# Kernel tuning notes

Hardware: AMD Instinct MI355X
Metric: run time of the kernel (lower is better)

Reference implementation:

```python
import jax, jax.numpy as jnp
import numpy as np

NY, NU, NHIDDEN = 64, 32, 512
T, BATCH = 512, 256
DAMP = 0.99


def setup_inputs() -> dict:
    key = jax.random.key(0)
    ks = jax.random.split(key, 8)
    nh2 = NHIDDEN // 2
    theta = jax.random.uniform(ks[0], (nh2,)) * (jnp.pi / 2)
    lmbd_real = DAMP * jnp.cos(theta)
    lmbd_imag = DAMP * jnp.sin(theta)
    B = jax.random.normal(ks[1], (NHIDDEN, NU)) / np.sqrt(NU) * np.sqrt(1.0 - DAMP ** 2)
    W_y2x = jax.random.normal(ks[2], (NHIDDEN, NY)) / np.sqrt(NY)
    b_y2x = jnp.zeros((NHIDDEN,), jnp.float32)
    W_x2y = jax.random.normal(ks[3], (NY, NHIDDEN)) / np.sqrt(NHIDDEN)
    b_x2y = jnp.zeros((NY,), jnp.float32)
    y0 = jax.random.normal(ks[4], (BATCH, NY), jnp.float32)
    U = jax.random.normal(ks[5], (T, BATCH, NU), jnp.float32)
    return {"y0": y0, "U": U, "lmbd_real": lmbd_real, "lmbd_imag": lmbd_imag,
            "B": B, "W_y2x": W_y2x, "b_y2x": b_y2x, "W_x2y": W_x2y, "b_x2y": b_x2y}


def reference(y0, U, lmbd_real, lmbd_imag, B, W_y2x, b_y2x, W_x2y, b_x2y):
    # x_{k+1} = x_k @ A^T + B u_k, where A = [[diag(lr), -diag(li)], [diag(li), diag(lr)]]
    # i.e. an elementwise complex rotation of the paired state halves.
    nh2 = lmbd_real.shape[0]
    Bu = jnp.einsum('tbu,hu->tbh', U, B)          # [T, batch, Nhidden]
    x0 = y0 @ W_y2x.T + b_y2x                     # [batch, Nhidden]

    def step(x, bu):
        xr, xi = x[..., :nh2], x[..., nh2:]
        nr = lmbd_real * xr - lmbd_imag * xi
        ni = lmbd_imag * xr + lmbd_real * xi
        xn = jnp.concatenate([nr, ni], axis=-1) + bu
        return xn, xn

    _, Xs = jax.lax.scan(step, x0, Bu)            # [T, batch, Nhidden]
    X = jnp.concatenate([x0[None], Xs], axis=0)   # [T+1, batch, Nhidden]
    Y = X @ W_x2y.T + b_x2y                       # [T+1, batch, Ny]
    return Y
```

## Files before the change

### kernel.cpp

```cpp
#include <hip/hip_runtime.h>


constexpr int NY  = 64;
constexpr int NU  = 32;
constexpr int NH  = 512;
constexpr int NH2 = 256;
constexpr int TT  = 512;
constexpr int BB  = 256;
constexpr int KK  = 16;
constexpr int NSS = TT / KK;

constexpr int USP = 40;
constexpr int BUP = 513;
constexpr int XSP = 520;

typedef __attribute__((ext_vector_type(4))) short sh4;
typedef __attribute__((ext_vector_type(8))) short sh8;
typedef __attribute__((ext_vector_type(4))) float f32x4;

#define MFMA16(a, b, c) __builtin_amdgcn_mfma_f32_16x16x32_bf16((a), (b), (c), 0, 0, 0)
#define CAT8(a, b) __builtin_shufflevector((a), (b), 0, 1, 2, 3, 4, 5, 6, 7)

__device__ __forceinline__ unsigned short bfh(float x) {
    return (unsigned short)(__float_as_uint(x) >> 16);
}
__device__ __forceinline__ float bf2f(unsigned short h) {
    return __uint_as_float(((unsigned)h) << 16);
}

__global__ __launch_bounds__(512, 2)
void lru_fused_kernel(const float* __restrict__ y0,
                      const float* __restrict__ U,
                      const float* __restrict__ lmr,
                      const float* __restrict__ lmi,
                      const float* __restrict__ Bmat,
                      const float* __restrict__ Wy2x,
                      const float* __restrict__ by2x,
                      const float* __restrict__ Wx2y,
                      const float* __restrict__ bx2y,
                      float* __restrict__ Y)
{
    const int b    = blockIdx.x;
    const int tid  = threadIdx.x;
    const int w    = tid >> 6;
    const int l    = tid & 63;
    const int lr16 = l & 15;
    const int lg   = l >> 4;

    __shared__ unsigned short us_h[2][64][USP], us_l[2][64][USP];
    __shared__ float          bu[KK][BUP];
    __shared__ unsigned short xs_h[KK][XSP], xs_l[KK][XSP];
    __shared__ float          psy[8][4][16][17];
    __shared__ float          y0s[NY];

    sh8 whi[4][2], wlo[4][2];
#pragma unroll
    for (int nt = 0; nt < 4; ++nt) {
#pragma unroll
        for (int kk2 = 0; kk2 < 2; ++kk2) {
            sh8 vh, vl;
#pragma unroll
            for (int h2 = 0; h2 < 2; ++h2) {
                const int k0 = (w << 6) + (kk2 << 5) + (h2 << 4) + (lg << 2);
                const int p0 = k0 >> 1;
                const float* Wn = Wx2y + ((nt << 4) + lr16) * NH;
                const float e[4] = { Wn[p0], Wn[p0 + 256], Wn[p0 + 1], Wn[p0 + 257] };
#pragma unroll
                for (int j = 0; j < 4; ++j) {
                    const unsigned short h = bfh(e[j]);
                    vh[h2 * 4 + j] = (short)h;
                    vl[h2 * 4 + j] = (short)bfh(e[j] - bf2f(h));
                }
            }
            whi[nt][kk2] = vh;
            wlo[nt][kk2] = vl;
        }
    }
    sh8 bbh[4], bbl[4];
#pragma unroll
    for (int q = 0; q < 4; ++q) {
        sh8 vh, vl;
#pragma unroll
        for (int h2 = 0; h2 < 2; ++h2) {
            const int hrow = (w << 6) + (q << 4) + lr16;
            const int u0   = (h2 << 4) + (lg << 2);
            const float4 f4 = *reinterpret_cast<const float4*>(&Bmat[hrow * NU + u0]);
            const float e[4] = { f4.x, f4.y, f4.z, f4.w };
#pragma unroll
            for (int j = 0; j < 4; ++j) {
                const unsigned short h = bfh(e[j]);
                vh[h2 * 4 + j] = (short)h;
                vl[h2 * 4 + j] = (short)bfh(e[j] - bf2f(h));
            }
        }
        bbh[q] = vh;
        bbl[q] = vl;
    }
    const float bias = bx2y[l];

    const float4* Ug = reinterpret_cast<const float4*>(U);
    {
        const int i = tid;
        const float4 f = Ug[((i >> 3) * BB + b) * 8 + (i & 7)];
        const int t = i >> 3, c4 = (i & 7) << 2;
        sh4 vh, vl;
        const float e[4] = { f.x, f.y, f.z, f.w };
#pragma unroll
        for (int j = 0; j < 4; ++j) {
            const unsigned short h = bfh(e[j]);
            vh[j] = (short)h;
            vl[j] = (short)bfh(e[j] - bf2f(h));
        }
        *reinterpret_cast<sh4*>(&us_h[0][t][c4]) = vh;
        *reinterpret_cast<sh4*>(&us_l[0][t][c4]) = vl;
    }
    if (tid < NY) y0s[tid] = y0[b * NY + tid];
    __syncthreads();

    float lamr = 0.f, lami = 0.f, xr = 0.f, xi = 0.f;
    if (tid < NH2) {
        lamr = lmr[tid];
        lami = lmi[tid];
        const float* wr = &Wy2x[tid * NY];
        const float* wi = &Wy2x[(NH2 + tid) * NY];
        float a0 = 0, a1 = 0, a2 = 0, a3 = 0;
        float c0 = 0, c1 = 0, c2 = 0, c3 = 0;
#pragma unroll
        for (int y = 0; y < NY; y += 4) {
            a0 += wr[y + 0] * y0s[y + 0];
            a1 += wr[y + 1] * y0s[y + 1];
            a2 += wr[y + 2] * y0s[y + 2];
            a3 += wr[y + 3] * y0s[y + 3];
            c0 += wi[y + 0] * y0s[y + 0];
            c1 += wi[y + 1] * y0s[y + 1];
            c2 += wi[y + 2] * y0s[y + 2];
            c3 += wi[y + 3] * y0s[y + 3];
        }
        xr = by2x[tid]       + (a0 + a1) + (a2 + a3);
        xi = by2x[NH2 + tid] + (c0 + c1) + (c2 + c3);
        const unsigned short hr = bfh(xr), hi2 = bfh(xi);
        reinterpret_cast<unsigned*>(&xs_h[0][0])[tid] = (unsigned)hr | ((unsigned)hi2 << 16);
        reinterpret_cast<unsigned*>(&xs_l[0][0])[tid] =
            (unsigned)bfh(xr - bf2f(hr)) | ((unsigned)bfh(xi - bf2f(hi2)) << 16);
    }
    __syncthreads();

    {
        f32x4 ay[4];
#pragma unroll
        for (int nt = 0; nt < 4; ++nt) ay[nt] = (f32x4){0.f, 0.f, 0.f, 0.f};
#pragma unroll
        for (int kk2 = 0; kk2 < 2; ++kk2) {
            const unsigned short* xp = &xs_h[lr16][(w << 6) + (kk2 << 5) + (lg << 2)];
            const unsigned short* xq = &xs_l[lr16][(w << 6) + (kk2 << 5) + (lg << 2)];
            const sh8 axh = CAT8(*(const sh4*)xp, *(const sh4*)(xp + 16));
            const sh8 axl = CAT8(*(const sh4*)xq, *(const sh4*)(xq + 16));
#pragma unroll
            for (int nt = 0; nt < 4; ++nt) {
                ay[nt] = MFMA16(axh, whi[nt][kk2], ay[nt]);
                ay[nt] = MFMA16(axl, whi[nt][kk2], ay[nt]);
                ay[nt] = MFMA16(axh, wlo[nt][kk2], ay[nt]);
            }
        }
#pragma unroll
        for (int nt = 0; nt < 4; ++nt)
#pragma unroll
            for (int r = 0; r < 4; ++r)
                psy[w][nt][(lg << 2) + r][lr16] = ay[nt][r];
    }
    __syncthreads();
    if (tid < NY) {
        float acc = bias;
#pragma unroll
        for (int w8 = 0; w8 < 8; ++w8) acc += psy[w8][l >> 4][0][l & 15];
        Y[b * NY + l] = acc;
    }

    float4 pf0, pf1;

    for (int st = 0; st < NSS; ++st) {
        const int c   = st >> 2;
        const int q4  = st & 3;
        const int buf = c & 1;

        if (q4 == 0 && c < 7 && tid >= NH2) {
            const int t0g = (c + 1) << 6;
            const int i0  = tid - NH2;
            const int i1  = tid;
            pf0 = Ug[((t0g + (i0 >> 3)) * BB + b) * 8 + (i0 & 7)];
            pf1 = Ug[((t0g + (i1 >> 3)) * BB + b) * 8 + (i1 & 7)];
        }

        {
            const int t0 = q4 << 4;
            const unsigned short* up = &us_h[buf][t0 + lr16][lg << 2];
            const unsigned short* uq = &us_l[buf][t0 + lr16][lg << 2];
            const sh8 auh = CAT8(*(const sh4*)up, *(const sh4*)(up + 16));
            const sh8 aul = CAT8(*(const sh4*)uq, *(const sh4*)(uq + 16));
#pragma unroll
            for (int q = 0; q < 4; ++q) {
                f32x4 acc = (f32x4){0.f, 0.f, 0.f, 0.f};
                acc = MFMA16(auh, bbh[q], acc);
                acc = MFMA16(auh, bbl[q], acc);
                acc = MFMA16(aul, bbh[q], acc);
                const int col = (w << 6) + (q << 4) + lr16;
#pragma unroll
                for (int r = 0; r < 4; ++r)
                    bu[(lg << 2) + r][col] = acc[r];
            }
        }
        __syncthreads();

        if (tid < NH2) {
#pragma unroll
            for (int k = 0; k < KK; ++k) {
                const float bur = bu[k][tid];
                const float bui = bu[k][NH2 + tid];
                const float nr = lamr * xr - lami * xi + bur;
                const float ni = lami * xr + lamr * xi + bui;
                xr = nr;
                xi = ni;
                const unsigned short hr = bfh(xr), hi2 = bfh(xi);
                reinterpret_cast<unsigned*>(&xs_h[k][0])[tid] =
                    (unsigned)hr | ((unsigned)hi2 << 16);
                reinterpret_cast<unsigned*>(&xs_l[k][0])[tid] =
                    (unsigned)bfh(xr - bf2f(hr)) | ((unsigned)bfh(xi - bf2f(hi2)) << 16);
            }
        } else if (q4 == 1 && c < 7) {
            const int nbuf = buf ^ 1;
#pragma unroll
            for (int v = 0; v < 2; ++v) {
                const float4 f = v ? pf1 : pf0;
                const int i = v ? tid : (tid - NH2);
                const int t = i >> 3, c4 = (i & 7) << 2;
                sh4 vh, vl;
                const float e[4] = { f.x, f.y, f.z, f.w };
#pragma unroll
                for (int j = 0; j < 4; ++j) {
                    const unsigned short h = bfh(e[j]);
                    vh[j] = (short)h;
                    vl[j] = (short)bfh(e[j] - bf2f(h));
                }
                *reinterpret_cast<sh4*>(&us_h[nbuf][t][c4]) = vh;
                *reinterpret_cast<sh4*>(&us_l[nbuf][t][c4]) = vl;
            }
        }
        __syncthreads();

        {
            f32x4 ay[4];
#pragma unroll
            for (int nt = 0; nt < 4; ++nt) ay[nt] = (f32x4){0.f, 0.f, 0.f, 0.f};
#pragma unroll
            for (int kk2 = 0; kk2 < 2; ++kk2) {
                const unsigned short* xp = &xs_h[lr16][(w << 6) + (kk2 << 5) + (lg << 2)];
                const unsigned short* xq = &xs_l[lr16][(w << 6) + (kk2 << 5) + (lg << 2)];
                const sh8 axh = CAT8(*(const sh4*)xp, *(const sh4*)(xp + 16));
                const sh8 axl = CAT8(*(const sh4*)xq, *(const sh4*)(xq + 16));
#pragma unroll
                for (int nt = 0; nt < 4; ++nt) {
                    ay[nt] = MFMA16(axh, whi[nt][kk2], ay[nt]);
                    ay[nt] = MFMA16(axl, whi[nt][kk2], ay[nt]);
                    ay[nt] = MFMA16(axh, wlo[nt][kk2], ay[nt]);
                }
            }
#pragma unroll
            for (int nt = 0; nt < 4; ++nt)
#pragma unroll
                for (int r = 0; r < 4; ++r)
                    psy[w][nt][(lg << 2) + r][lr16] = ay[nt][r];
        }
        __syncthreads();

        {
#pragma unroll
            for (int rep = 0; rep < 2; ++rep) {
                const int mm = w + (rep << 3);
                float acc = bias;
#pragma unroll
                for (int w8 = 0; w8 < 8; ++w8)
                    acc += psy[w8][l >> 4][mm][l & 15];
                const int s = (st << 4) + mm + 1;
                Y[(s * BB + b) * NY + l] = acc;
            }
        }
    }
}

extern "C" void kernel_launch(void* const* d_in, const int* in_sizes, int n_in,
                              void* d_out, int out_size, void* d_ws, size_t ws_size,
                              hipStream_t stream) {
    const float* y0   = (const float*)d_in[0];
    const float* U    = (const float*)d_in[1];
    const float* lmr  = (const float*)d_in[2];
    const float* lmi  = (const float*)d_in[3];
    const float* Bm   = (const float*)d_in[4];
    const float* Wy2x = (const float*)d_in[5];
    const float* by2x = (const float*)d_in[6];
    const float* Wx2y = (const float*)d_in[7];
    const float* bx2y = (const float*)d_in[8];
    float* Y = (float*)d_out;

    lru_fused_kernel<<<dim3(BB), dim3(512), 0, stream>>>(
        y0, U, lmr, lmi, Bm, Wy2x, by2x, Wx2y, bx2y, Y);
}
```

Before: 167.0 us.

## Specialize warps into scan/Bu producers and output-GEMM consumers with double-buffered state

Splits the 8 warps into two roles. Warps 0-3 compute the Bu GEMM and run the serial complex recurrence. Warps 4-7 hold all Wx2y fragments in registers, compute the output projection for the previous 16-step chunk from a double-buffered xs, and handle U prefetch and conversion. The loop drops from three barriers per step to two, lets the output GEMM overlap with the next scan chunk, and permutes the LDS layouts so fragments load as single 8-wide reads. The cost is a larger register footprint per warp (32 fragment vectors), an extra pipeline drain iteration, and more LDS for the doubled xs buffers.

Result: no change. 163.8 us (-1.9%).

```diff
diff --git a/kernel.cpp b/kernel.cpp
--- a/kernel.cpp
+++ b/kernel.cpp
@@ -11,21 +11,30 @@
 constexpr int NSS = TT / KK;
 
 constexpr int USP = 40;
-constexpr int BUP = 513;
-constexpr int XSP = 520;
+constexpr int XSP = 544;
+constexpr int BUP = 516;
+constexpr int PSP = 20;
 
 typedef __attribute__((ext_vector_type(4))) short sh4;
 typedef __attribute__((ext_vector_type(8))) short sh8;
 typedef __attribute__((ext_vector_type(4))) float f32x4;
 
 #define MFMA16(a, b, c) __builtin_amdgcn_mfma_f32_16x16x32_bf16((a), (b), (c), 0, 0, 0)
-#define CAT8(a, b) __builtin_shufflevector((a), (b), 0, 1, 2, 3, 4, 5, 6, 7)
 
 __device__ __forceinline__ unsigned short bfh(float x) {
     return (unsigned short)(__float_as_uint(x) >> 16);
 }
 __device__ __forceinline__ float bf2f(unsigned short h) {
     return __uint_as_float(((unsigned)h) << 16);
+}
+__device__ __forceinline__ void cvt4(const float4 f, sh4& vh, sh4& vl) {
+    const float e[4] = { f.x, f.y, f.z, f.w };
+#pragma unroll
+    for (int j = 0; j < 4; ++j) {
+        const unsigned short h = bfh(e[j]);
+        vh[j] = (short)h;
+        vl[j] = (short)bfh(e[j] - bf2f(h));
+    }
 }
 
 __global__ __launch_bounds__(512, 2)
@@ -48,79 +57,79 @@
     const int lg   = l >> 4;
 
     __shared__ unsigned short us_h[2][64][USP], us_l[2][64][USP];
+    __shared__ unsigned short xs_h[2][KK][XSP], xs_l[2][KK][XSP];
     __shared__ float          bu[KK][BUP];
-    __shared__ unsigned short xs_h[KK][XSP], xs_l[KK][XSP];
-    __shared__ float          psy[8][4][16][17];
+    __shared__ float          psy[4][2][16][PSP];
     __shared__ float          y0s[NY];
 
-    sh8 whi[4][2], wlo[4][2];
-#pragma unroll
-    for (int nt = 0; nt < 4; ++nt) {
-#pragma unroll
-        for (int kk2 = 0; kk2 < 2; ++kk2) {
+    sh8 frg[32];
+    float lamr = 0.f, lami = 0.f, xr = 0.f, xi = 0.f;
+    float biasE = 0.f;
+    int   xwrd  = 0;
+
+    if (tid < NH2) {
+#pragma unroll
+        for (int q = 0; q < 8; ++q) {
             sh8 vh, vl;
 #pragma unroll
             for (int h2 = 0; h2 < 2; ++h2) {
-                const int k0 = (w << 6) + (kk2 << 5) + (h2 << 4) + (lg << 2);
-                const int p0 = k0 >> 1;
-                const float* Wn = Wx2y + ((nt << 4) + lr16) * NH;
-                const float e[4] = { Wn[p0], Wn[p0 + 256], Wn[p0 + 1], Wn[p0 + 257] };
-#pragma unroll
-                for (int j = 0; j < 4; ++j) {
-                    const unsigned short h = bfh(e[j]);
-                    vh[h2 * 4 + j] = (short)h;
-                    vl[h2 * 4 + j] = (short)bfh(e[j] - bf2f(h));
-                }
-            }
-            whi[nt][kk2] = vh;
-            wlo[nt][kk2] = vl;
-        }
-    }
-    sh8 bbh[4], bbl[4];
-#pragma unroll
-    for (int q = 0; q < 4; ++q) {
-        sh8 vh, vl;
-#pragma unroll
-        for (int h2 = 0; h2 < 2; ++h2) {
-            const int hrow = (w << 6) + (q << 4) + lr16;
-            const int u0   = (h2 << 4) + (lg << 2);
-            const float4 f4 = *reinterpret_cast<const float4*>(&Bmat[hrow * NU + u0]);
-            const float e[4] = { f4.x, f4.y, f4.z, f4.w };
-#pragma unroll
-            for (int j = 0; j < 4; ++j) {
-                const unsigned short h = bfh(e[j]);
-                vh[h2 * 4 + j] = (short)h;
-                vl[h2 * 4 + j] = (short)bfh(e[j] - bf2f(h));
-            }
-        }
-        bbh[q] = vh;
-        bbl[q] = vl;
-    }
-    const float bias = bx2y[l];
+                const int hrow = (w << 7) + (q << 4) + lr16;
+                const int u0   = (h2 << 4) + (lg << 2);
+                const float4 f4 = *reinterpret_cast<const float4*>(&Bmat[hrow * NU + u0]);
+                sh4 th, tl;
+                cvt4(f4, th, tl);
+#pragma unroll
+                for (int j = 0; j < 4; ++j) { vh[h2 * 4 + j] = th[j]; vl[h2 * 4 + j] = tl[j]; }
+            }
+            frg[q] = vh;
+            frg[8 + q] = vl;
+        }
+        lamr = lmr[tid];
+        lami = lmi[tid];
+        const int q_ = tid & 15, blk = tid >> 4;
+        xwrd = blk * 16 + ((q_ & 7) >> 1) * 4 + (q_ >> 3) * 2 + (q_ & 1);
+    } else {
+        const int j = w - 4, ntp = j >> 1, kh = j & 1;
+#pragma unroll
+        for (int ntt = 0; ntt < 2; ++ntt) {
+            const int n = ((ntp << 1) + ntt) * 16 + lr16;
+            const float* Wn = Wx2y + n * NH;
+#pragma unroll
+            for (int ks = 0; ks < 8; ++ks) {
+                sh8 vh, vl;
+#pragma unroll
+                for (int h2 = 0; h2 < 2; ++h2) {
+                    const int k0 = (kh << 8) + (ks << 5) + (h2 << 4) + (lg << 2);
+                    const int p0 = k0 >> 1;
+                    const float e[4] = { Wn[p0], Wn[p0 + 256], Wn[p0 + 1], Wn[p0 + 257] };
+#pragma unroll
+                    for (int j2 = 0; j2 < 4; ++j2) {
+                        const unsigned short h = bfh(e[j2]);
+                        vh[h2 * 4 + j2] = (short)h;
+                        vl[h2 * 4 + j2] = (short)bfh(e[j2] - bf2f(h));
+                    }
+                }
+                frg[ntt * 8 + ks] = vh;
+                frg[16 + ntt * 8 + ks] = vl;
+            }
+        }
+        biasE = bx2y[(j << 4) + lr16];
+    }
 
     const float4* Ug = reinterpret_cast<const float4*>(U);
     {
-        const int i = tid;
-        const float4 f = Ug[((i >> 3) * BB + b) * 8 + (i & 7)];
-        const int t = i >> 3, c4 = (i & 7) << 2;
+        const int i = tid, t = i >> 3, g = i & 7;
+        const float4 f = Ug[((t * BB + b) << 3) + g];
+        const int pos = (g < 4) ? (g << 3) : (((g - 4) << 3) + 4);
         sh4 vh, vl;
-        const float e[4] = { f.x, f.y, f.z, f.w };
-#pragma unroll
-        for (int j = 0; j < 4; ++j) {
-            const unsigned short h = bfh(e[j]);
-            vh[j] = (short)h;
-            vl[j] = (short)bfh(e[j] - bf2f(h));
-        }
-        *reinterpret_cast<sh4*>(&us_h[0][t][c4]) = vh;
-        *reinterpret_cast<sh4*>(&us_l[0][t][c4]) = vl;
+        cvt4(f, vh, vl);
+        *reinterpret_cast<sh4*>(&us_h[0][t][pos]) = vh;
+        *reinterpret_cast<sh4*>(&us_l[0][t][pos]) = vl;
     }
     if (tid < NY) y0s[tid] = y0[b * NY + tid];
     __syncthreads();
 
-    float lamr = 0.f, lami = 0.f, xr = 0.f, xi = 0.f;
     if (tid < NH2) {
-        lamr = lmr[tid];
-        lami = lmi[tid];
         const float* wr = &Wy2x[tid * NY];
         const float* wi = &Wy2x[(NH2 + tid) * NY];
         float a0 = 0, a1 = 0, a2 = 0, a3 = 0;
@@ -139,151 +148,113 @@
         xr = by2x[tid]       + (a0 + a1) + (a2 + a3);
         xi = by2x[NH2 + tid] + (c0 + c1) + (c2 + c3);
         const unsigned short hr = bfh(xr), hi2 = bfh(xi);
-        reinterpret_cast<unsigned*>(&xs_h[0][0])[tid] = (unsigned)hr | ((unsigned)hi2 << 16);
-        reinterpret_cast<unsigned*>(&xs_l[0][0])[tid] =
+        reinterpret_cast<unsigned*>(&xs_h[1][0][0])[xwrd] =
+            (unsigned)hr | ((unsigned)hi2 << 16);
+        reinterpret_cast<unsigned*>(&xs_l[1][0][0])[xwrd] =
             (unsigned)bfh(xr - bf2f(hr)) | ((unsigned)bfh(xi - bf2f(hi2)) << 16);
     }
     __syncthreads();
 
-    {
-        f32x4 ay[4];
-#pragma unroll
-        for (int nt = 0; nt < 4; ++nt) ay[nt] = (f32x4){0.f, 0.f, 0.f, 0.f};
-#pragma unroll
-        for (int kk2 = 0; kk2 < 2; ++kk2) {
-            const unsigned short* xp = &xs_h[lr16][(w << 6) + (kk2 << 5) + (lg << 2)];
-            const unsigned short* xq = &xs_l[lr16][(w << 6) + (kk2 << 5) + (lg << 2)];
-            const sh8 axh = CAT8(*(const sh4*)xp, *(const sh4*)(xp + 16));
-            const sh8 axl = CAT8(*(const sh4*)xq, *(const sh4*)(xq + 16));
-#pragma unroll
-            for (int nt = 0; nt < 4; ++nt) {
-                ay[nt] = MFMA16(axh, whi[nt][kk2], ay[nt]);
-                ay[nt] = MFMA16(axl, whi[nt][kk2], ay[nt]);
-                ay[nt] = MFMA16(axh, wlo[nt][kk2], ay[nt]);
-            }
-        }
-#pragma unroll
-        for (int nt = 0; nt < 4; ++nt)
-#pragma unroll
-            for (int r = 0; r < 4; ++r)
-                psy[w][nt][(lg << 2) + r][lr16] = ay[nt][r];
-    }
-    __syncthreads();
-    if (tid < NY) {
-        float acc = bias;
-#pragma unroll
-        for (int w8 = 0; w8 < 8; ++w8) acc += psy[w8][l >> 4][0][l & 15];
-        Y[b * NY + l] = acc;
-    }
-
     float4 pf0, pf1;
 
-    for (int st = 0; st < NSS; ++st) {
-        const int c   = st >> 2;
-        const int q4  = st & 3;
-        const int buf = c & 1;
-
-        if (q4 == 0 && c < 7 && tid >= NH2) {
-            const int t0g = (c + 1) << 6;
-            const int i0  = tid - NH2;
-            const int i1  = tid;
-            pf0 = Ug[((t0g + (i0 >> 3)) * BB + b) * 8 + (i0 & 7)];
-            pf1 = Ug[((t0g + (i1 >> 3)) * BB + b) * 8 + (i1 & 7)];
-        }
-
-        {
-            const int t0 = q4 << 4;
-            const unsigned short* up = &us_h[buf][t0 + lr16][lg << 2];
-            const unsigned short* uq = &us_l[buf][t0 + lr16][lg << 2];
-            const sh8 auh = CAT8(*(const sh4*)up, *(const sh4*)(up + 16));
-            const sh8 aul = CAT8(*(const sh4*)uq, *(const sh4*)(uq + 16));
-#pragma unroll
-            for (int q = 0; q < 4; ++q) {
-                f32x4 acc = (f32x4){0.f, 0.f, 0.f, 0.f};
-                acc = MFMA16(auh, bbh[q], acc);
-                acc = MFMA16(auh, bbl[q], acc);
-                acc = MFMA16(aul, bbh[q], acc);
-                const int col = (w << 6) + (q << 4) + lr16;
-#pragma unroll
-                for (int r = 0; r < 4; ++r)
-                    bu[(lg << 2) + r][col] = acc[r];
+    for (int st = 0; st <= NSS; ++st) {
+        if (tid < NH2) {
+            if (st < NSS) {
+                const int su = (st >> 2) & 1, t0 = (st & 3) << 4;
+                const sh8 auh = *reinterpret_cast<const sh8*>(&us_h[su][t0 + lr16][lg << 3]);
+                const sh8 aul = *reinterpret_cast<const sh8*>(&us_l[su][t0 + lr16][lg << 3]);
+#pragma unroll
+                for (int q = 0; q < 8; ++q) {
+                    f32x4 acc = (f32x4){0.f, 0.f, 0.f, 0.f};
+                    acc = MFMA16(auh, frg[q], acc);
+                    acc = MFMA16(aul, frg[q], acc);
+                    acc = MFMA16(auh, frg[8 + q], acc);
+                    const int h = (w << 7) + (q << 4) + lr16;
+#pragma unroll
+                    for (int r = 0; r < 4; ++r)
+                        bu[(lg << 2) + r][h] = acc[r];
+                }
+            }
+        } else {
+            const int c = st >> 2;
+            if ((st & 3) == 0 && c < 7 && st < NSS) {
+                const int i0 = tid - NH2, i1 = tid;
+                pf0 = Ug[(((((c + 1) << 6) + (i0 >> 3)) * BB + b) << 3) + (i0 & 7)];
+                pf1 = Ug[(((((c + 1) << 6) + (i1 >> 3)) * BB + b) << 3) + (i1 & 7)];
+            }
+            const int sx = (st + 1) & 1;
+            const int j = w - 4, kh = j & 1;
+            f32x4 a0 = (f32x4){0.f, 0.f, 0.f, 0.f};
+            f32x4 a1 = (f32x4){0.f, 0.f, 0.f, 0.f};
+#pragma unroll
+            for (int ks = 0; ks < 8; ++ks) {
+                const int sp = (kh << 8) + (ks << 5) + (lg << 3);
+                const sh8 axh = *reinterpret_cast<const sh8*>(&xs_h[sx][lr16][sp]);
+                const sh8 axl = *reinterpret_cast<const sh8*>(&xs_l[sx][lr16][sp]);
+                a0 = MFMA16(axh, frg[ks], a0);
+                a0 = MFMA16(axl, frg[ks], a0);
+                a0 = MFMA16(axh, frg[16 + ks], a0);
+                a1 = MFMA16(axh, frg[8 + ks], a1);
+                a1 = MFMA16(axl, frg[8 + ks], a1);
+                a1 = MFMA16(axh, frg[24 + ks], a1);
+            }
+#pragma unroll
+            for (int r = 0; r < 4; ++r) {
+                psy[j][0][(lg << 2) + r][lr16] = a0[r];
+                psy[j][1][(lg << 2) + r][lr16] = a1[r];
             }
         }
         __syncthreads();
 
         if (tid < NH2) {
-#pragma unroll
-            for (int k = 0; k < KK; ++k) {
-                const float bur = bu[k][tid];
-                const float bui = bu[k][NH2 + tid];
-                const float nr = lamr * xr - lami * xi + bur;
-                const float ni = lami * xr + lamr * xi + bui;
-                xr = nr;
-                xi = ni;
-                const unsigned short hr = bfh(xr), hi2 = bfh(xi);
-                reinterpret_cast<unsigned*>(&xs_h[k][0])[tid] =
-                    (unsigned)hr | ((unsigned)hi2 << 16);
-                reinterpret_cast<unsigned*>(&xs_l[k][0])[tid] =
-                    (unsigned)bfh(xr - bf2f(hr)) | ((unsigned)bfh(xi - bf2f(hi2)) << 16);
-            }
-        } else if (q4 == 1 && c < 7) {
-            const int nbuf = buf ^ 1;
-#pragma unroll
-            for (int v = 0; v < 2; ++v) {
-                const float4 f = v ? pf1 : pf0;
-                const int i = v ? tid : (tid - NH2);
-                const int t = i >> 3, c4 = (i & 7) << 2;
-                sh4 vh, vl;
-                const float e[4] = { f.x, f.y, f.z, f.w };
-#pragma unroll
-                for (int j = 0; j < 4; ++j) {
-                    const unsigned short h = bfh(e[j]);
-                    vh[j] = (short)h;
-                    vl[j] = (short)bfh(e[j] - bf2f(h));
-                }
-                *reinterpret_cast<sh4*>(&us_h[nbuf][t][c4]) = vh;
-                *reinterpret_cast<sh4*>(&us_l[nbuf][t][c4]) = vl;
+            if (st < NSS) {
+                const int sw = st & 1;
+                unsigned* xh = reinterpret_cast<unsigned*>(&xs_h[sw][0][0]);
+                unsigned* xl = reinterpret_cast<unsigned*>(&xs_l[sw][0][0]);
+#pragma unroll
+                for (int k = 0; k < KK; ++k) {
+                    const float bur = bu[k][tid];
+                    const float bui = bu[k][NH2 + tid];
+                    const float nr = lamr * xr - lami * xi + bur;
+                    const float ni = lami * xr + lamr * xi + bui;
+                    xr = nr;
+                    xi = ni;
+                    const unsigned short hr = bfh(xr), hi2 = bfh(xi);
+                    xh[k * (XSP / 2) + xwrd] = (unsigned)hr | ((unsigned)hi2 << 16);
+                    xl[k * (XSP / 2) + xwrd] =
+                        (unsigned)bfh(xr - bf2f(hr)) | ((unsigned)bfh(xi - bf2f(hi2)) << 16);
+                }
+            }
+        } else {
+            if ((st & 3) == 1 && (st >> 2) < 7) {
+                const int ns = ((st >> 2) + 1) & 1;
+#pragma unroll
+                for (int v = 0; v < 2; ++v) {
+                    const float4 f = v ? pf1 : pf0;
+                    const int i = v ? tid : (tid - NH2);
+                    const int t = i >> 3, g = i & 7;
+                    const int pos = (g < 4) ? (g << 3) : (((g - 4) << 3) + 4);
+                    sh4 vh, vl;
+                    cvt4(f, vh, vl);
+                    *reinterpret_cast<sh4*>(&us_h[ns][t][pos]) = vh;
+                    *reinterpret_cast<sh4*>(&us_l[ns][t][pos]) = vl;
+                }
+            }
+            const int j = w - 4;
+            const int j0 = j & ~1;
+#pragma unroll
+            for (int r = 0; r < 4; ++r) {
+                const int m = (lg << 2) + r;
+                const float v = psy[j0][j & 1][m][lr16] + psy[j0 + 1][j & 1][m][lr16] + biasE;
+                if (st == 0) {
+                    if (m == 0) Y[b * NY + (j << 4) + lr16] = v;
+                } else {
+                    const int s = ((st - 1) << 4) + m + 1;
+                    Y[(s * BB + b) * NY + (j << 4) + lr16] = v;
+                }
             }
         }
         __syncthreads();
-
-        {
-            f32x4 ay[4];
-#pragma unroll
-            for (int nt = 0; nt < 4; ++nt) ay[nt] = (f32x4){0.f, 0.f, 0.f, 0.f};
-#pragma unroll
-            for (int kk2 = 0; kk2 < 2; ++kk2) {
-                const unsigned short* xp = &xs_h[lr16][(w << 6) + (kk2 << 5) + (lg << 2)];
-                const unsigned short* xq = &xs_l[lr16][(w << 6) + (kk2 << 5) + (lg << 2)];
-                const sh8 axh = CAT8(*(const sh4*)xp, *(const sh4*)(xp + 16));
-                const sh8 axl = CAT8(*(const sh4*)xq, *(const sh4*)(xq + 16));
-#pragma unroll
-                for (int nt = 0; nt < 4; ++nt) {
-                    ay[nt] = MFMA16(axh, whi[nt][kk2], ay[nt]);
-                    ay[nt] = MFMA16(axl, whi[nt][kk2], ay[nt]);
-                    ay[nt] = MFMA16(axh, wlo[nt][kk2], ay[nt]);
-                }
-            }
-#pragma unroll
-            for (int nt = 0; nt < 4; ++nt)
-#pragma unroll
-                for (int r = 0; r < 4; ++r)
-                    psy[w][nt][(lg << 2) + r][lr16] = ay[nt][r];
-        }
-        __syncthreads();
-
-        {
-#pragma unroll
-            for (int rep = 0; rep < 2; ++rep) {
-                const int mm = w + (rep << 3);
-                float acc = bias;
-#pragma unroll
-                for (int w8 = 0; w8 < 8; ++w8)
-                    acc += psy[w8][l >> 4][mm][l & 15];
-                const int s = (st << 4) + mm + 1;
-                Y[(s * BB + b) * NY + l] = acc;
-            }
-        }
     }
 }
 
```
